# Kernel optimization log

Measured on AMD Instinct MI355X. Metric: run time of the kernel, lower is better.

Reference implementation:

```python
import jax, jax.numpy as jnp
import numpy as np


def _gcn_conv(x, src, dst, num_nodes, W, b):
    """PyG GCNConv: add self-loops, symmetric normalization, scatter-add, bias."""
    h = x @ W  # [N, F_out]
    # degree over destination nodes (all edge weights are 1, incl. self-loops)
    deg = jax.ops.segment_sum(jnp.ones_like(dst, dtype=h.dtype), dst,
                              num_segments=num_nodes)
    deg_inv_sqrt = jnp.where(deg > 0, jax.lax.rsqrt(deg), 0.0)
    norm = deg_inv_sqrt[src] * deg_inv_sqrt[dst]  # [E+N]
    msg = h[src] * norm[:, None]                  # gather + scale
    out = jax.ops.segment_sum(msg, dst, num_segments=num_nodes)  # scatter-add
    return out + b


def setup_inputs() -> dict:
    key = jax.random.key(0)
    k_x, k_e, k_w1, k_w2 = jax.random.split(key, 4)
    N, E, F = 50000, 800000, 128
    x = jax.random.normal(k_x, (N, F), dtype=jnp.float32)
    edge_index = jax.random.randint(k_e, (2, E), 0, N, dtype=jnp.int64)
    scale = 1.0 / np.sqrt(F)
    W1 = jax.random.normal(k_w1, (F, F), dtype=jnp.float32) * scale
    b1 = jnp.zeros((F,), dtype=jnp.float32)
    W2 = jax.random.normal(k_w2, (F, F), dtype=jnp.float32) * scale
    b2 = jnp.zeros((F,), dtype=jnp.float32)
    return {"x": x, "edge_index": edge_index, "W1": W1, "b1": b1,
            "W2": W2, "b2": b2}


def reference(x, edge_index, W1, b1, W2, b2):
    num_nodes = x.shape[0]
    loops = jnp.arange(num_nodes, dtype=edge_index.dtype)
    src = jnp.concatenate([edge_index[0], loops])
    dst = jnp.concatenate([edge_index[1], loops])
    # layer 1: GCNConv -> Identity norm -> relu -> dropout(eval=identity)
    h = jax.nn.relu(_gcn_conv(x, src, dst, num_nodes, W1, b1))
    # layer 2 (last_activation=True, so relu again)
    out = jax.nn.relu(_gcn_conv(h, src, dst, num_nodes, W2, b2))
    return out
```

## Files before the change

### kernel.cpp

```cpp
#include <hip/hip_runtime.h>
#include <hip/hip_bf16.h>

#define CDIV(a,b) (((a)+(b)-1)/(b))

typedef __bf16 bf16x8 __attribute__((ext_vector_type(8)));
typedef float  f32x4  __attribute__((ext_vector_type(4)));

union Frag16 { uint4 u; bf16x8 f; unsigned short s[8]; };
union Pack8  { unsigned short s[4]; uint2 u; };

__device__ __forceinline__ unsigned short f2bf(float f) {
    unsigned u = __float_as_uint(f);
    return (unsigned short)((u + 0x7fff + ((u >> 16) & 1)) >> 16);
}
__device__ __forceinline__ float bf2f(unsigned short s) {
    return __uint_as_float(((unsigned)s) << 16);
}

__device__ __forceinline__ int load_src(const int* e, int f, int E, int i) {
    return f ? e[i] : e[2 * i];
}
__device__ __forceinline__ int load_dst(const int* e, int f, int E, int i) {
    return f ? e[E + i] : e[2 * (E + i)];
}

__global__ __launch_bounds__(256) void prep_kernel(const float* __restrict__ W1,
                                                   const float* __restrict__ W2,
                                                   unsigned short* __restrict__ Wf1h,
                                                   unsigned short* __restrict__ Wf1l,
                                                   unsigned short* __restrict__ Wf2h,
                                                   unsigned short* __restrict__ Wf2l,
                                                   const int* __restrict__ edges,
                                                   int* __restrict__ flag, int E) {
    int tid = threadIdx.x;
    if (blockIdx.x == 2) {
        int n = min(E, 4096);
        int found = 0;
        for (int j = tid; j < n; j += 256) found |= (edges[2 * j + 1] != 0);
        if (found) *flag = 1;
        return;
    }
    const float* W = (blockIdx.x == 0) ? W1 : W2;
    unsigned short* Wfh = (blockIdx.x == 0) ? Wf1h : Wf2h;
    unsigned short* Wfl = (blockIdx.x == 0) ? Wf1l : Wf2l;
    #pragma unroll
    for (int it = 0; it < 8; ++it) {
        int c = it * 256 + tid;
        int ntk = c >> 6;
        int lane = c & 63;
        int ks = ntk & 3;
        int ntile = ntk >> 2;
        int quad = lane >> 4, nlo = lane & 15;
        int n = ntile * 16 + nlo;
        Frag16 h, l;
        #pragma unroll
        for (int j = 0; j < 8; ++j) {
            float w = W[(ks * 32 + quad * 8 + j) * 128 + n];
            h.s[j] = f2bf(w);
            float rr = w - bf2f(h.s[j]);
            l.s[j] = f2bf(rr);
        }
        *(uint4*)(Wfh + (size_t)c * 8) = h.u;
        *(uint4*)(Wfl + (size_t)c * 8) = l.u;
    }
}

__device__ __forceinline__ void gemm_body(const float* __restrict__ X,
                                          const unsigned short* __restrict__ Wfh,
                                          const unsigned short* __restrict__ Wfl,
                                          unsigned short* __restrict__ out16,
                                          int N, int blk,
                                          unsigned short (*Xh)[136],
                                          unsigned short (*Xl)[136]) {
    int tid = threadIdx.x;
    int row0 = blk * 64;
    #pragma unroll
    for (int it = 0; it < 8; ++it) {
        int f = it * 256 + tid;
        int r = f >> 5, c4 = f & 31;
        float4 v = make_float4(0.f, 0.f, 0.f, 0.f);
        int gr = row0 + r;
        if (gr < N) v = *(const float4*)(X + (size_t)gr * 128 + c4 * 4);
        float vv[4] = {v.x, v.y, v.z, v.w};
        Pack8 h, l;
        #pragma unroll
        for (int j = 0; j < 4; ++j) {
            h.s[j] = f2bf(vv[j]);
            float rr = vv[j] - bf2f(h.s[j]);
            l.s[j] = f2bf(rr);
        }
        *(uint2*)(&Xh[r][c4 * 4]) = h.u;
        *(uint2*)(&Xl[r][c4 * 4]) = l.u;
    }
    __syncthreads();

    int lane = tid & 63;
    int wv = tid >> 6;
    int quad = lane >> 4, nlo = lane & 15;
    f32x4 acc[8];
    #pragma unroll
    for (int t = 0; t < 8; ++t) acc[t] = (f32x4){0.f, 0.f, 0.f, 0.f};

    #pragma unroll
    for (int ks = 0; ks < 4; ++ks) {
        int kcol = ks * 32 + quad * 8;
        Frag16 xh, xl;
        xh.u = *(const uint4*)(&Xh[wv * 16 + nlo][kcol]);
        xl.u = *(const uint4*)(&Xl[wv * 16 + nlo][kcol]);
        #pragma unroll
        for (int t = 0; t < 8; ++t) {
            size_t cidx = ((size_t)(t * 4 + ks) * 64 + lane) * 8;
            Frag16 wh, wl;
            wh.u = *(const uint4*)(Wfh + cidx);
            wl.u = *(const uint4*)(Wfl + cidx);
            acc[t] = __builtin_amdgcn_mfma_f32_16x16x32_bf16(xh.f, wh.f, acc[t], 0, 0, 0);
            acc[t] = __builtin_amdgcn_mfma_f32_16x16x32_bf16(xh.f, wl.f, acc[t], 0, 0, 0);
            acc[t] = __builtin_amdgcn_mfma_f32_16x16x32_bf16(xl.f, wh.f, acc[t], 0, 0, 0);
        }
    }
    #pragma unroll
    for (int rg = 0; rg < 4; ++rg) {
        int gr = row0 + wv * 16 + quad * 4 + rg;
        if (gr < N) {
            #pragma unroll
            for (int t = 0; t < 8; ++t)
                out16[(size_t)gr * 128 + t * 16 + nlo] = f2bf(acc[t][rg]);
        }
    }
}

__global__ __launch_bounds__(256) void fat_kernel(const float* __restrict__ X,
                                                  const unsigned short* __restrict__ Wfh,
                                                  const unsigned short* __restrict__ Wfl,
                                                  unsigned short* __restrict__ out16,
                                                  int N, int Ggemm,
                                                  const int* __restrict__ edges,
                                                  const int* __restrict__ flag,
                                                  int* __restrict__ counts_sh,
                                                  int* __restrict__ rank, int E) {
    __shared__ unsigned short Xh[64][136];
    __shared__ unsigned short Xl[64][136];
    if (blockIdx.x < (unsigned)Ggemm) {
        gemm_body(X, Wfh, Wfl, out16, N, blockIdx.x, Xh, Xl);
        return;
    }
    int e = (blockIdx.x - Ggemm) * 256 + threadIdx.x;
    if (e >= E) return;
    int f = *flag;
    int d = load_dst(edges, f, E, e);
    int s = blockIdx.x & 7;
    int r = atomicAdd(&counts_sh[s * N + d], 1);
    rank[e] = (r << 3) | s;
}

__global__ __launch_bounds__(256) void gemm_mfma_kernel(const float* __restrict__ X,
                                                        const unsigned short* __restrict__ Wfh,
                                                        const unsigned short* __restrict__ Wfl,
                                                        unsigned short* __restrict__ out16,
                                                        int N) {
    __shared__ unsigned short Xh[64][136];
    __shared__ unsigned short Xl[64][136];
    gemm_body(X, Wfh, Wfl, out16, N, blockIdx.x, Xh, Xl);
}

__global__ __launch_bounds__(256) void merge_dis_kernel(int* __restrict__ counts_sh,
                                                        int* __restrict__ counts,
                                                        float* __restrict__ dis,
                                                        int* __restrict__ bsum, int N) {
    __shared__ int red[4];
    int tid = threadIdx.x;
    int bs = 0;
    #pragma unroll
    for (int j = 0; j < 4; ++j) {
        int d = blockIdx.x * 1024 + j * 256 + tid;
        if (d < N) {
            int run = 0;
            #pragma unroll
            for (int s = 0; s < 8; ++s) {
                int v = counts_sh[s * N + d];
                counts_sh[s * N + d] = run;
                run += v;
            }
            counts[d] = run;
            dis[d] = rsqrtf((float)(run + 1));
            bs += run;
        }
    }
    #pragma unroll
    for (int off = 32; off >= 1; off >>= 1) bs += __shfl_down(bs, off, 64);
    if ((tid & 63) == 0) red[tid >> 6] = bs;
    __syncthreads();
    if (tid == 0) bsum[blockIdx.x] = red[0] + red[1] + red[2] + red[3];
}

__global__ void scan2_kernel(const int* __restrict__ bsum, int* __restrict__ boff,
                             int B, int* __restrict__ row_ptr, int N, int E) {
    int lane = threadIdx.x;
    int carry = 0;
    for (int base = 0; base < B; base += 64) {
        int i = base + lane;
        int v = (i < B) ? bsum[i] : 0;
        int x = v;
        #pragma unroll
        for (int off = 1; off < 64; off <<= 1) {
            int t = __shfl_up(x, off, 64);
            if (lane >= off) x += t;
        }
        if (i < B) boff[i] = carry + x - v;
        carry += __shfl(x, 63, 64);
    }
    if (lane == 0) row_ptr[N] = E;
}

__global__ __launch_bounds__(256) void scan3_kernel(const int* __restrict__ counts,
                                                    const int* __restrict__ boff,
                                                    int* __restrict__ row_ptr, int N) {
    __shared__ int wsum[4];
    int tid = threadIdx.x;
    int lane = tid & 63, wv = tid >> 6;
    int base = blockIdx.x * 1024 + tid * 4;
    int c[4];
    #pragma unroll
    for (int j = 0; j < 4; ++j) c[j] = (base + j < N) ? counts[base + j] : 0;
    int tsum = c[0] + c[1] + c[2] + c[3];
    int x = tsum;
    #pragma unroll
    for (int off = 1; off < 64; off <<= 1) {
        int t = __shfl_up(x, off, 64);
        if (lane >= off) x += t;
    }
    int texcl = x - tsum;
    if (lane == 63) wsum[wv] = x;
    __syncthreads();
    int woff = 0;
    for (int w = 0; w < wv; ++w) woff += wsum[w];
    int off0 = boff[blockIdx.x] + woff + texcl;
    int run = 0;
    #pragma unroll
    for (int j = 0; j < 4; ++j) {
        if (base + j < N) row_ptr[base + j] = off0 + run;
        run += c[j];
    }
}

__global__ void fill_kernel(const int* __restrict__ edges, const int* __restrict__ flag,
                            const int* __restrict__ row_ptr, const int* __restrict__ rank,
                            const int* __restrict__ counts_sh,
                            const float* __restrict__ dis, int2* __restrict__ edata,
                            int E, int N) {
    int e = blockIdx.x * blockDim.x + threadIdx.x;
    if (e >= E) return;
    int f = *flag;
    int s = load_src(edges, f, E, e);
    int d = load_dst(edges, f, E, e);
    int rk = rank[e];
    int sh = rk & 7;
    int pos = row_ptr[d] + counts_sh[sh * N + d] + (rk >> 3);
    edata[pos] = make_int2(s, __float_as_int(dis[s]));
}

__global__ __launch_bounds__(256) void agg_kernel(const unsigned short* __restrict__ H16,
                                                  const int* __restrict__ row_ptr,
                                                  const int2* __restrict__ edata,
                                                  const float* __restrict__ dis,
                                                  const float* __restrict__ bias,
                                                  float* __restrict__ out, int N) {
    int wid = (blockIdx.x * blockDim.x + threadIdx.x) >> 6;
    int lane = threadIdx.x & 63;
    if (wid >= N) return;
    const ushort2* H2 = (const ushort2*)H16;
    float dd = dis[wid];
    ushort2 hv = H2[(size_t)wid * 64 + lane];
    float wself = dd * dd;
    float2 acc = make_float2(bf2f(hv.x) * wself, bf2f(hv.y) * wself);
    int e0 = __builtin_amdgcn_readfirstlane(row_ptr[wid]);
    int e1 = __builtin_amdgcn_readfirstlane(row_ptr[wid + 1]);
    for (int e = e0; e < e1; e += 8) {
        int rem = e1 - e;
        int   sj[8];
        float wj[8];
        #pragma unroll
        for (int j = 0; j < 8; ++j) {
            bool valid = j < rem;
            int2 ed = edata[valid ? e + j : e];
            sj[j] = ed.x;
            wj[j] = valid ? __int_as_float(ed.y) * dd : 0.f;
        }
        ushort2 aj[8];
        #pragma unroll
        for (int j = 0; j < 8; ++j)
            aj[j] = H2[(size_t)sj[j] * 64 + lane];
        #pragma unroll
        for (int j = 0; j < 8; ++j) {
            acc.x += bf2f(aj[j].x) * wj[j];
            acc.y += bf2f(aj[j].y) * wj[j];
        }
    }
    float2 b = ((const float2*)bias)[lane];
    float2 o = make_float2(fmaxf(acc.x + b.x, 0.f), fmaxf(acc.y + b.y, 0.f));
    ((float2*)out)[(size_t)wid * 64 + lane] = o;
}

extern "C" void kernel_launch(void* const* d_in, const int* in_sizes, int n_in,
                              void* d_out, int out_size, void* d_ws, size_t ws_size,
                              hipStream_t stream) {
    const float* x    = (const float*)d_in[0];
    const int*  edges = (const int*)d_in[1];
    const float* W1   = (const float*)d_in[2];
    const float* b1   = (const float*)d_in[3];
    const float* W2   = (const float*)d_in[4];
    const float* b2   = (const float*)d_in[5];
    float* out = (float*)d_out;

    const int F = 128;
    const int N = in_sizes[0] / F;
    const int E = in_sizes[1] / 2;
    const int NB = CDIV(N, 1024);
    const int Ggemm = CDIV(N, 64);
    const int Gcount = CDIV(E, 256);

    #define AL4(v) (((v) + 3) & ~3)
    unsigned short* A16 = (unsigned short*)d_ws;
    float* B        = (float*)(A16 + (size_t)AL4(N * F));
    float* dis      = B + (size_t)AL4(N * F);
    int*  counts    = (int*)(dis + AL4(N));
    int*  counts_sh = counts + AL4(N);
    int*  flag      = counts_sh + AL4(8 * N);
    int*  row_ptr   = flag + 4;
    int*  bsum      = row_ptr + AL4(N + 1);
    int*  boff      = bsum + 64;
    int*  rank      = boff + 64;
    int2* edata     = (int2*)(rank + AL4(E));
    unsigned short* Wf1h = (unsigned short*)(edata + E);
    unsigned short* Wf1l = Wf1h + 16384;
    unsigned short* Wf2h = Wf1l + 16384;
    unsigned short* Wf2l = Wf2h + 16384;

    hipMemsetAsync(counts_sh, 0, ((size_t)AL4(8 * N) + 4) * sizeof(int), stream);

    prep_kernel<<<3, 256, 0, stream>>>(W1, W2, Wf1h, Wf1l, Wf2h, Wf2l, edges, flag, E);
    fat_kernel<<<Ggemm + Gcount, 256, 0, stream>>>(x, Wf1h, Wf1l, A16, N, Ggemm,
                                                   edges, flag, counts_sh, rank, E);
    merge_dis_kernel<<<NB, 256, 0, stream>>>(counts_sh, counts, dis, bsum, N);
    scan2_kernel<<<1, 64, 0, stream>>>(bsum, boff, NB, row_ptr, N, E);
    scan3_kernel<<<NB, 256, 0, stream>>>(counts, boff, row_ptr, N);
    fill_kernel<<<Gcount, 256, 0, stream>>>(edges, flag, row_ptr, rank,
                                            counts_sh, dis, edata, E, N);

    agg_kernel<<<CDIV(N * 64, 256), 256, 0, stream>>>(A16, row_ptr, edata, dis, b1, B, N);
    gemm_mfma_kernel<<<CDIV(N, 64), 256, 0, stream>>>(B, Wf2h, Wf2l, A16, N);
    agg_kernel<<<CDIV(N * 64, 256), 256, 0, stream>>>(A16, row_ptr, edata, dis, b2, out, N);
}
```

Before: 229.5 us.

## Store layer-1 activations in bf16 and fold memset into prep kernel

The first aggregation now writes its ReLU output as bf16 instead of fp32. A new second-layer GEMM reads those bf16 rows straight into MFMA fragments, using only the split hi/lo weights and skipping the LDS hi/lo split of the activations. The separate hipMemsetAsync that zeroed the counts is replaced by extra blocks in the prep kernel, which saves an API call and a dispatch. This halves the intermediate memory traffic, at the cost of bf16 rounding of the hidden activations and therefore lower precision than the previous hi/lo split.

```diff
diff --git a/kernel.cpp b/kernel.cpp
--- a/kernel.cpp
+++ b/kernel.cpp
@@ -31,13 +31,21 @@
                                                    unsigned short* __restrict__ Wf2h,
                                                    unsigned short* __restrict__ Wf2l,
                                                    const int* __restrict__ edges,
-                                                   int* __restrict__ flag, int E) {
+                                                   int* __restrict__ flag, int E,
+                                                   int4* __restrict__ zero_base, int Z4) {
     int tid = threadIdx.x;
     if (blockIdx.x == 2) {
+        if (tid == 0) *flag = 0;
+        __syncthreads();
         int n = min(E, 4096);
         int found = 0;
         for (int j = tid; j < n; j += 256) found |= (edges[2 * j + 1] != 0);
         if (found) *flag = 1;
+        return;
+    }
+    if (blockIdx.x >= 3) {
+        int idx = (blockIdx.x - 3) * 256 + tid;
+        if (idx < Z4) zero_base[idx] = make_int4(0, 0, 0, 0);
         return;
     }
     const float* W = (blockIdx.x == 0) ? W1 : W2;
@@ -153,14 +161,46 @@
     rank[e] = (r << 3) | s;
 }
 
-__global__ __launch_bounds__(256) void gemm_mfma_kernel(const float* __restrict__ X,
-                                                        const unsigned short* __restrict__ Wfh,
-                                                        const unsigned short* __restrict__ Wfl,
-                                                        unsigned short* __restrict__ out16,
-                                                        int N) {
-    __shared__ unsigned short Xh[64][136];
-    __shared__ unsigned short Xl[64][136];
-    gemm_body(X, Wfh, Wfl, out16, N, blockIdx.x, Xh, Xl);
+__global__ __launch_bounds__(256) void gemm_h1_kernel(const unsigned short* __restrict__ H1,
+                                                      const unsigned short* __restrict__ Wfh,
+                                                      const unsigned short* __restrict__ Wfl,
+                                                      unsigned short* __restrict__ out16,
+                                                      int N) {
+    int tid = threadIdx.x;
+    int lane = tid & 63, wv = tid >> 6;
+    int quad = lane >> 4, nlo = lane & 15;
+    int row0 = blockIdx.x * 64 + wv * 16;
+    int arow = min(row0 + nlo, N - 1);
+    Frag16 xa[4];
+    #pragma unroll
+    for (int ks = 0; ks < 4; ++ks)
+        xa[ks].u = *(const uint4*)(H1 + (size_t)arow * 128 + ks * 32 + quad * 8);
+
+    f32x4 acc[8];
+    #pragma unroll
+    for (int t = 0; t < 8; ++t) acc[t] = (f32x4){0.f, 0.f, 0.f, 0.f};
+
+    #pragma unroll
+    for (int ks = 0; ks < 4; ++ks) {
+        #pragma unroll
+        for (int t = 0; t < 8; ++t) {
+            size_t cidx = ((size_t)(t * 4 + ks) * 64 + lane) * 8;
+            Frag16 wh, wl;
+            wh.u = *(const uint4*)(Wfh + cidx);
+            wl.u = *(const uint4*)(Wfl + cidx);
+            acc[t] = __builtin_amdgcn_mfma_f32_16x16x32_bf16(xa[ks].f, wh.f, acc[t], 0, 0, 0);
+            acc[t] = __builtin_amdgcn_mfma_f32_16x16x32_bf16(xa[ks].f, wl.f, acc[t], 0, 0, 0);
+        }
+    }
+    #pragma unroll
+    for (int rg = 0; rg < 4; ++rg) {
+        int gr = row0 + quad * 4 + rg;
+        if (gr < N) {
+            #pragma unroll
+            for (int t = 0; t < 8; ++t)
+                out16[(size_t)gr * 128 + t * 16 + nlo] = f2bf(acc[t][rg]);
+        }
+    }
 }
 
 __global__ __launch_bounds__(256) void merge_dis_kernel(int* __restrict__ counts_sh,
@@ -259,12 +299,13 @@
     edata[pos] = make_int2(s, __float_as_int(dis[s]));
 }
 
+template <bool BF16OUT>
 __global__ __launch_bounds__(256) void agg_kernel(const unsigned short* __restrict__ H16,
                                                   const int* __restrict__ row_ptr,
                                                   const int2* __restrict__ edata,
                                                   const float* __restrict__ dis,
                                                   const float* __restrict__ bias,
-                                                  float* __restrict__ out, int N) {
+                                                  void* __restrict__ outp, int N) {
     int wid = (blockIdx.x * blockDim.x + threadIdx.x) >> 6;
     int lane = threadIdx.x & 63;
     if (wid >= N) return;
@@ -297,8 +338,14 @@
         }
     }
     float2 b = ((const float2*)bias)[lane];
-    float2 o = make_float2(fmaxf(acc.x + b.x, 0.f), fmaxf(acc.y + b.y, 0.f));
-    ((float2*)out)[(size_t)wid * 64 + lane] = o;
+    float ox = fmaxf(acc.x + b.x, 0.f);
+    float oy = fmaxf(acc.y + b.y, 0.f);
+    if (BF16OUT) {
+        ushort2 o = make_ushort2(f2bf(ox), f2bf(oy));
+        ((ushort2*)outp)[(size_t)wid * 64 + lane] = o;
+    } else {
+        ((float2*)outp)[(size_t)wid * 64 + lane] = make_float2(ox, oy);
+    }
 }
 
 extern "C" void kernel_launch(void* const* d_in, const int* in_sizes, int n_in,
@@ -321,8 +368,8 @@
 
     #define AL4(v) (((v) + 3) & ~3)
     unsigned short* A16 = (unsigned short*)d_ws;
-    float* B        = (float*)(A16 + (size_t)AL4(N * F));
-    float* dis      = B + (size_t)AL4(N * F);
+    unsigned short* H1  = A16 + (size_t)AL4(N * F);
+    float* dis      = (float*)(H1 + (size_t)AL4(N * F));
     int*  counts    = (int*)(dis + AL4(N));
     int*  counts_sh = counts + AL4(N);
     int*  flag      = counts_sh + AL4(8 * N);
@@ -336,9 +383,11 @@
     unsigned short* Wf2h = Wf1l + 16384;
     unsigned short* Wf2l = Wf2h + 16384;
 
-    hipMemsetAsync(counts_sh, 0, ((size_t)AL4(8 * N) + 4) * sizeof(int), stream);
-
-    prep_kernel<<<3, 256, 0, stream>>>(W1, W2, Wf1h, Wf1l, Wf2h, Wf2l, edges, flag, E);
+    const int Z4 = AL4(8 * N) / 4;
+    const int Gprep = 3 + CDIV(Z4, 256);
+
+    prep_kernel<<<Gprep, 256, 0, stream>>>(W1, W2, Wf1h, Wf1l, Wf2h, Wf2l,
+                                           edges, flag, E, (int4*)counts_sh, Z4);
     fat_kernel<<<Ggemm + Gcount, 256, 0, stream>>>(x, Wf1h, Wf1l, A16, N, Ggemm,
                                                    edges, flag, counts_sh, rank, E);
     merge_dis_kernel<<<NB, 256, 0, stream>>>(counts_sh, counts, dis, bsum, N);
@@ -347,7 +396,7 @@
     fill_kernel<<<Gcount, 256, 0, stream>>>(edges, flag, row_ptr, rank,
                                             counts_sh, dis, edata, E, N);
 
-    agg_kernel<<<CDIV(N * 64, 256), 256, 0, stream>>>(A16, row_ptr, edata, dis, b1, B, N);
-    gemm_mfma_kernel<<<CDIV(N, 64), 256, 0, stream>>>(B, Wf2h, Wf2l, A16, N);
-    agg_kernel<<<CDIV(N * 64, 256), 256, 0, stream>>>(A16, row_ptr, edata, dis, b2, out, N);
-}
+    agg_kernel<true><<<CDIV(N * 64, 256), 256, 0, stream>>>(A16, row_ptr, edata, dis, b1, H1, N);
+    gemm_h1_kernel<<<CDIV(N, 64), 256, 0, stream>>>(H1, Wf2h, Wf2l, A16, N);
+    agg_kernel<false><<<CDIV(N * 64, 256), 256, 0, stream>>>(A16, row_ptr, edata, dis, b2, out, N);
+}
```

Measured after the change: 224.9 us. -2.0%, faster.
